# Kernel tuning notes

Measured on AMD Instinct MI355X. Metric: run time of the kernel, lower is better.

The kernel has to match this reference:

```python
import jax, jax.numpy as jnp
import numpy as np
import itertools

N = 600000
CIN = 64
COUT = 64
KS = 3
STRIDE = 2
DIL = 1
GRID = 256        # coordinate range before striding
M = 512           # per-axis key radix (fits int32 keys for batch<=2)
SHIFT = (KS - 1) // 2 * DIL   # keeps shifted coords non-negative under neighbor offsets
SENT = 2 ** 30    # sentinel key for padded unique slots
BN_EPS = 1e-5

OFFSETS = list(itertools.product(range(-(KS // 2), KS // 2 + 1), repeat=3))  # 27 offsets, row-major


def setup_inputs() -> dict:
    key = jax.random.key(0)
    k1, k2, k3, k4, k5, k6, k7, k8 = jax.random.split(key, 8)
    xyz = jax.random.randint(k1, (N, 3), 0, GRID, dtype=jnp.int32)
    b = jax.random.randint(k2, (N, 1), 0, 2, dtype=jnp.int32)  # batch of 2 scenes
    coords = jnp.concatenate([xyz, b], axis=1)                 # [N,4] = (x,y,z,batch)
    feats = jax.random.normal(k3, (N, CIN), dtype=jnp.float32)
    weight = jax.random.normal(k4, (27, CIN, COUT), dtype=jnp.float32) / np.sqrt(27 * CIN)
    bn_scale = jax.random.uniform(k5, (COUT,), jnp.float32, 0.5, 1.5)
    bn_bias = jax.random.normal(k6, (COUT,), jnp.float32) * 0.1
    bn_mean = jax.random.normal(k7, (COUT,), jnp.float32) * 0.1
    bn_var = jax.random.uniform(k8, (COUT,), jnp.float32, 0.5, 1.5)
    return {"coords": coords, "feats": feats, "weight": weight,
            "bn_scale": bn_scale, "bn_bias": bn_bias, "bn_mean": bn_mean, "bn_var": bn_var}


def _encode(xyz, b):
    # pack (batch, x, y, z) into a single sortable int32 key
    return ((b * M + xyz[:, 0] + SHIFT) * M + (xyz[:, 1] + SHIFT)) * M + (xyz[:, 2] + SHIFT)


def _forward(coords, feats, weight, bn_scale, bn_bias, bn_mean, bn_var):
    # --- stride path: voxel downsample via unique + scatter-add (index_add) ---
    xyz = coords[:, :3] // STRIDE
    b = coords[:, 3]
    keys = _encode(xyz, b)                                   # [N]
    ukeys, inv = jnp.unique(keys, size=N, fill_value=SENT, return_inverse=True)  # sorted, padded
    fds = jax.ops.segment_sum(feats, inv, num_segments=N)    # pooled feats [N, CIN]
    valid = ukeys < SENT                                      # real (non-padded) voxels

    # --- sparse 3x3x3 conv at stride 1 (output coords == input coords) ---
    # gather(neighbor) -> matmul(W_k) -> accumulate, per kernel offset
    out = jnp.zeros((N, COUT), dtype=feats.dtype)
    for k, (dx, dy, dz) in enumerate(OFFSETS):
        delta = ((dx * M) + dy) * M + dz
        q = ukeys + delta * DIL
        pos = jnp.clip(jnp.searchsorted(ukeys, q), 0, N - 1)
        match = (ukeys[pos] == q) & valid
        gathered = jnp.where(match[:, None], fds[pos], 0.0)   # [N, CIN]
        out = out + gathered @ weight[k]

    # --- BatchNorm (eval-mode running stats) + ReLU ---
    inv_std = jax.lax.rsqrt(bn_var + BN_EPS)
    out = (out - bn_mean) * (bn_scale * inv_std) + bn_bias
    out = jax.nn.relu(out)
    return jnp.where(valid[:, None], out, 0.0)                # zero padded rows


def reference(coords, feats, weight, bn_scale, bn_bias, bn_mean, bn_var):
    return _forward(coords, feats, weight, bn_scale, bn_bias, bn_mean, bn_var)
```

## Files before the change

kernel.cpp:

```cpp
#include <hip/hip_runtime.h>
#include <hip/hip_bf16.h>

#define NPTS 600000
#define NKEYS (1 << 22)
#define CHUNK 4096
#define NPART (NKEYS / CHUNK)

typedef unsigned int u32;
typedef unsigned short u16;
typedef __attribute__((ext_vector_type(8))) short short8;
typedef __attribute__((ext_vector_type(4))) float f32x4;

__device__ __forceinline__ u16 f2bf(float x) {
  union { float f; u32 u; } c; c.f = x;
  u32 r = c.u + 0x7fffu + ((c.u >> 16) & 1u);
  return (u16)(r >> 16);
}

__global__ void k0a_bn(const float* __restrict__ s, const float* __restrict__ b,
                       const float* __restrict__ m, const float* __restrict__ v,
                       float* __restrict__ ab) {
  int c = threadIdx.x;
  float a = s[c] * rsqrtf(v[c] + 1e-5f);
  ab[c] = a;
  ab[64 + c] = b[c] - m[c] * a;
}

__global__ void k0b_wt(const float* __restrict__ W, u16* __restrict__ Wt) {
  int e = blockIdx.x * 256 + threadIdx.x;
  if (e >= 27 * 4096) return;
  int k = e >> 12, rem = e & 4095, cin = rem >> 6, cout = rem & 63;
  Wt[(k << 12) + (cout << 6) + cin] = f2bf(W[e]);
}

__global__ void k1_keys(const int* __restrict__ coords, int* __restrict__ keys,
                        u32* __restrict__ lut) {
  int i = blockIdx.x * 256 + threadIdx.x;
  if (i >= NPTS) return;
  int4 c4 = *(const int4*)(coords + i * 4);
  int k = (c4.w << 21) | ((c4.x >> 1) << 14) | ((c4.y >> 1) << 7) | (c4.z >> 1);
  keys[i] = k;
  atomicAdd(&lut[k], 1u);
}

__global__ void k2a_part(const u32* __restrict__ lut, u32* __restrict__ partials) {
  __shared__ u32 sd[256];
  int blk = blockIdx.x, t = threadIdx.x;
  const u32* p = lut + blk * CHUNK;
  u32 s = 0;
  for (int j = t; j < CHUNK; j += 256) s += (p[j] != 0u);
  sd[t] = s; __syncthreads();
  for (int o = 128; o > 0; o >>= 1) { if (t < o) sd[t] += sd[t + o]; __syncthreads(); }
  if (t == 0) partials[blk] = sd[0];
}

__global__ void k2b_top(u32* __restrict__ partials) {
  __shared__ u32 sh[NPART];
  int t = threadIdx.x;
  u32 x = partials[t];
  sh[t] = x; __syncthreads();
  for (int off = 1; off < NPART; off <<= 1) {
    u32 add = (t >= off) ? sh[t - off] : 0u;
    __syncthreads();
    sh[t] += add;
    __syncthreads();
  }
  partials[t] = sh[t] - x;
  if (t == NPART - 1) partials[NPART] = sh[t];
}

__global__ void k2c_fill(u32* __restrict__ lut, const u32* __restrict__ partials,
                         int* __restrict__ r2k, float* __restrict__ fds32) {
  __shared__ u32 tsum[256];
  int blk = blockIdx.x, t = threadIdx.x;
  int base = blk * CHUNK + t * 16;
  u32 loc[16]; u32 s = 0;
#pragma unroll
  for (int j = 0; j < 16; j++) { loc[j] = lut[base + j]; s += (loc[j] != 0u); }
  tsum[t] = s; __syncthreads();
  for (int off = 1; off < 256; off <<= 1) {
    u32 add = (t >= off) ? tsum[t - off] : 0u;
    __syncthreads();
    tsum[t] += add;
    __syncthreads();
  }
  u32 rank = partials[blk] + tsum[t] - s;
#pragma unroll
  for (int j = 0; j < 16; j++) {
    if (loc[j]) {
      u32 flag = (loc[j] > 1u) ? 0x80000000u : 0u;
      lut[base + j] = (rank + 1u) | flag;
      r2k[rank] = base + j;
      if (flag) {
        float4 z = {0.f, 0.f, 0.f, 0.f};
        float* d = fds32 + ((size_t)rank << 6);
#pragma unroll
        for (int c = 0; c < 16; c++) *(float4*)(d + c * 4) = z;
      }
      rank++;
    } else lut[base + j] = 0u;
  }
}

__global__ void k3_seg(const float* __restrict__ feats, const int* __restrict__ keys,
                       const u32* __restrict__ lut, float* __restrict__ fds32,
                       u16* __restrict__ fdsb) {
  int idx = blockIdx.x * 256 + threadIdx.x;
  if (idx >= NPTS * 16) return;
  int i = idx >> 4, q = (idx & 15) << 2;
  u32 lv = lut[keys[i]];
  u32 r = (lv & 0x7fffffffu) - 1u;
  float4 v = *(const float4*)(feats + (size_t)i * 64 + q);
  if (lv >> 31) {
    float* dst = fds32 + ((size_t)r << 6) + q;
    atomicAdd(dst + 0, v.x); atomicAdd(dst + 1, v.y);
    atomicAdd(dst + 2, v.z); atomicAdd(dst + 3, v.w);
  } else {
    ushort4 o;
    o.x = f2bf(v.x); o.y = f2bf(v.y); o.z = f2bf(v.z); o.w = f2bf(v.w);
    *(ushort4*)(fdsb + ((size_t)r << 6) + q) = o;
  }
}

__global__ void k3b_fix(const int* __restrict__ r2k, const u32* __restrict__ lut,
                        const u32* __restrict__ pU,
                        const float* __restrict__ fds32, u16* __restrict__ fdsb) {
  int idx = blockIdx.x * 256 + threadIdx.x;
  int r = idx >> 2;
  if (r >= (int)(*pU)) return;
  u32 lv = lut[r2k[r]];
  if (!(lv >> 31)) return;
  int q = (idx & 3) << 4;
  const float* src = fds32 + ((size_t)r << 6) + q;
  u16* dst = fdsb + ((size_t)r << 6) + q;
#pragma unroll
  for (int j = 0; j < 4; j++) {
    float4 v = *(const float4*)(src + j * 4);
    ushort4 o;
    o.x = f2bf(v.x); o.y = f2bf(v.y); o.z = f2bf(v.z); o.w = f2bf(v.w);
    *(ushort4*)(dst + j * 4) = o;
  }
}

__global__ __launch_bounds__(320) void k4_conv(
    const u32* __restrict__ lut, const int* __restrict__ r2k,
    const u16* __restrict__ fdsb, const u16* __restrict__ Wt,
    const u32* __restrict__ pU, const float* __restrict__ ab,
    float* __restrict__ out) {
  __shared__ __align__(16) char ldsA[2][8192];
  const u32 U = *pU;
  int tid = threadIdx.x;
  int w = tid >> 6, l = tid & 63;
  int bid = blockIdx.x;
  int cpx = (int)gridDim.x >> 3;
  int swz = (bid & 7) * cpx + (bid >> 3);
  int rbase = swz * 64;

  int key = -1, x = 0, y = 0, z = 0;
  if (w == 0) {
    int r = rbase + l;
    key = ((u32)r < U) ? r2k[r] : -1;
    z = key & 127; y = (key >> 7) & 127; x = (key >> 14) & 127;
  }
  auto probe = [&](int k) -> u32 {
    int dx = k / 9 - 1, dy = (k / 3) % 3 - 1, dz = k % 3 - 1;
    int nx = x + dx, ny = y + dy, nz = z + dz;
    bool ok = (key >= 0) & ((u32)nx < 128u) & ((u32)ny < 128u) & ((u32)nz < 128u);
    int a = ok ? (key + dx * 16384 + dy * 128 + dz) : NKEYS;
    return lut[a];
  };
  auto gather = [&](int slot, u32 lvv) {
    u32 row = lvv ? ((lvv & 0x7fffffffu) - 1u) : (u32)NPTS;
    const u16* fr = fdsb + ((size_t)row << 6);
    char* dst = &ldsA[slot][l * 128];
    int r7 = l & 7;
#pragma unroll
    for (int j = 0; j < 8; j++) {
      short8 v = *(const short8*)(fr + j * 8);
      *(short8*)(dst + (((j + r7) & 7) << 4)) = v;
    }
  };

  int ct = w - 1;
  int col = l & 15, kg = l >> 4;
  f32x4 acc[4] = {};

  u32 lv_cur = 0;
  if (w == 0) {
    lv_cur = probe(0);
    gather(0, lv_cur);
    lv_cur = probe(1);
  }
  __syncthreads();

  for (int k = 0; k < 27; k++) {
    if (w == 0) {
      if (k + 1 < 27) {
        gather((k + 1) & 1, lv_cur);
        if (k + 2 < 27) lv_cur = probe(k + 2);
      }
    } else {
      const u16* wk = Wt + (k << 12) + (((ct << 4) + col) << 6) + (kg << 3);
      short8 b0 = *(const short8*)(wk);
      short8 b1 = *(const short8*)(wk + 32);
      const char* slab = &ldsA[k & 1][0];
#pragma unroll
      for (int rt = 0; rt < 4; rt++) {
        int row = (rt << 4) + col;
        const char* rp = slab + row * 128;
        int r7 = row & 7;
        short8 a0 = *(const short8*)(rp + (((kg + r7) & 7) << 4));
        short8 a1 = *(const short8*)(rp + (((kg + 4 + r7) & 7) << 4));
        acc[rt] = __builtin_amdgcn_mfma_f32_16x16x32_bf16(a0, b0, acc[rt], 0, 0, 0);
        acc[rt] = __builtin_amdgcn_mfma_f32_16x16x32_bf16(a1, b1, acc[rt], 0, 0, 0);
      }
    }
    __syncthreads();
  }

  if (w > 0) {
    int c = (ct << 4) | col;
    float al = ab[c], be = ab[64 + c];
#pragma unroll
    for (int rt = 0; rt < 4; rt++) {
#pragma unroll
      for (int i = 0; i < 4; i++) {
        int r = rbase + (rt << 4) + (kg << 2) + i;
        if (r >= NPTS) continue;
        bool valid = ((u32)r < U);
        float vv = 0.f;
        if (valid) {
          vv = fmaf(acc[rt][i], al, be);
          vv = vv > 0.f ? vv : 0.f;
        }
        out[((size_t)r << 6) + c] = vv;
      }
    }
  }
}

extern "C" void kernel_launch(void* const* d_in, const int* in_sizes, int n_in,
                              void* d_out, int out_size, void* d_ws, size_t ws_size,
                              hipStream_t stream) {
  const int*   coords = (const int*)d_in[0];
  const float* feats  = (const float*)d_in[1];
  const float* W      = (const float*)d_in[2];
  const float* bns    = (const float*)d_in[3];
  const float* bnb    = (const float*)d_in[4];
  const float* bnm    = (const float*)d_in[5];
  const float* bnv    = (const float*)d_in[6];
  float* out = (float*)d_out;

  char* ws = (char*)d_ws;
  size_t off = 0;
  auto alloc = [&](size_t bytes) -> void* {
    void* p = ws + off;
    off += (bytes + 255) & ~(size_t)255;
    return p;
  };
  u32* lut      = (u32*)alloc((size_t)(NKEYS + 1) * 4);
  u32* partials = (u32*)alloc((NPART + 8) * 4);
  int* keys     = (int*)alloc((size_t)NPTS * 4);
  int* r2k      = (int*)alloc((size_t)NPTS * 4);
  u16* fdsb     = (u16*)alloc((size_t)(NPTS + 1) * 64 * 2);
  u16* Wt       = (u16*)alloc((size_t)27 * 4096 * 2);
  float* ab     = (float*)alloc(128 * 4);
  (void)ws_size; (void)out_size; (void)n_in; (void)in_sizes;

  float* fds32 = out;

  hipMemsetAsync(lut, 0, (size_t)(NKEYS + 1) * 4, stream);
  hipMemsetAsync(fdsb + (size_t)NPTS * 64, 0, 128, stream);

  k0a_bn<<<1, 64, 0, stream>>>(bns, bnb, bnm, bnv, ab);
  k0b_wt<<<(27 * 4096 + 255) / 256, 256, 0, stream>>>(W, Wt);
  k1_keys<<<(NPTS + 255) / 256, 256, 0, stream>>>(coords, keys, lut);
  k2a_part<<<NPART, 256, 0, stream>>>(lut, partials);
  k2b_top<<<1, NPART, 0, stream>>>(partials);
  k2c_fill<<<NPART, 256, 0, stream>>>(lut, partials, r2k, fds32);
  k3_seg<<<(NPTS * 16 + 255) / 256, 256, 0, stream>>>(feats, keys, lut, fds32, fdsb);
  k3b_fix<<<(NPTS * 4 + 255) / 256, 256, 0, stream>>>(r2k, lut, partials + NPART, fds32, fdsb);
  k4_conv<<<(NPTS + 63) / 64, 320, 0, stream>>>(lut, r2k, fdsb, Wt,
                                                partials + NPART, ab, out);
}
```

Baseline: 538.3 us.

## Gather neighbor rows via direct global-to-LDS loads and use 2x2 warp tiling

The producer wave now copies gathered neighbor feature rows straight into LDS with global_load_lds, using a column-major chunk layout (1 KB per 16-byte chunk index). Before, each lane loaded 8 short8 values into registers and wrote them to a swizzled row-major LDS buffer. The four compute waves are rearranged from one 16-column tile over 64 rows each into a 2x2 tiling of 32 rows by 32 columns, which halves the A-fragment LDS reads per wave but doubles the weight loads. Launch bounds now ask for 6 blocks per CU to raise occupancy, at the risk of register pressure from the larger accumulator set.

```diff
diff --git a/kernel.cpp b/kernel.cpp
--- a/kernel.cpp
+++ b/kernel.cpp
@@ -142,7 +142,7 @@
   }
 }
 
-__global__ __launch_bounds__(320) void k4_conv(
+__global__ __launch_bounds__(320, 6) void k4_conv(
     const u32* __restrict__ lut, const int* __restrict__ r2k,
     const u16* __restrict__ fdsb, const u16* __restrict__ Wt,
     const u32* __restrict__ pU, const float* __restrict__ ab,
@@ -171,24 +171,22 @@
   };
   auto gather = [&](int slot, u32 lvv) {
     u32 row = lvv ? ((lvv & 0x7fffffffu) - 1u) : (u32)NPTS;
-    const u16* fr = fdsb + ((size_t)row << 6);
-    char* dst = &ldsA[slot][l * 128];
-    int r7 = l & 7;
-#pragma unroll
-    for (int j = 0; j < 8; j++) {
-      short8 v = *(const short8*)(fr + j * 8);
-      *(short8*)(dst + (((j + r7) & 7) << 4)) = v;
-    }
+    const char* fr = (const char*)(fdsb + ((size_t)row << 6));
+    char* slab = &ldsA[slot][0];
+#define GL(J) __builtin_amdgcn_global_load_lds( \
+      (const __attribute__((address_space(1))) void*)(fr + (J) * 16), \
+      (__attribute__((address_space(3))) void*)(slab + (J) * 1024), 16, 0, 0);
+    GL(0) GL(1) GL(2) GL(3) GL(4) GL(5) GL(6) GL(7)
+#undef GL
   };
 
-  int ct = w - 1;
+  int wi = (w - 1) >> 1, wj = (w - 1) & 1;
   int col = l & 15, kg = l >> 4;
-  f32x4 acc[4] = {};
+  f32x4 acc[2][2] = {};
 
   u32 lv_cur = 0;
   if (w == 0) {
-    lv_cur = probe(0);
-    gather(0, lv_cur);
+    gather(0, probe(0));
     lv_cur = probe(1);
   }
   __syncthreads();
@@ -200,40 +198,52 @@
         if (k + 2 < 27) lv_cur = probe(k + 2);
       }
     } else {
-      const u16* wk = Wt + (k << 12) + (((ct << 4) + col) << 6) + (kg << 3);
-      short8 b0 = *(const short8*)(wk);
-      short8 b1 = *(const short8*)(wk + 32);
+      const u16* wk = Wt + (k << 12);
+      short8 bf[2][2];
+#pragma unroll
+      for (int ct = 0; ct < 2; ct++)
+#pragma unroll
+        for (int h = 0; h < 2; h++)
+          bf[ct][h] = *(const short8*)(wk + (((wj << 5) + (ct << 4) + col) << 6) + (h << 5) + (kg << 3));
       const char* slab = &ldsA[k & 1][0];
-#pragma unroll
-      for (int rt = 0; rt < 4; rt++) {
-        int row = (rt << 4) + col;
-        const char* rp = slab + row * 128;
-        int r7 = row & 7;
-        short8 a0 = *(const short8*)(rp + (((kg + r7) & 7) << 4));
-        short8 a1 = *(const short8*)(rp + (((kg + 4 + r7) & 7) << 4));
-        acc[rt] = __builtin_amdgcn_mfma_f32_16x16x32_bf16(a0, b0, acc[rt], 0, 0, 0);
-        acc[rt] = __builtin_amdgcn_mfma_f32_16x16x32_bf16(a1, b1, acc[rt], 0, 0, 0);
-      }
+      short8 af[2][2];
+#pragma unroll
+      for (int rt = 0; rt < 2; rt++) {
+        int row = (wi << 5) + (rt << 4) + col;
+#pragma unroll
+        for (int h = 0; h < 2; h++)
+          af[rt][h] = *(const short8*)(slab + ((kg + (h << 2)) << 10) + (row << 4));
+      }
+#pragma unroll
+      for (int rt = 0; rt < 2; rt++)
+#pragma unroll
+        for (int ct = 0; ct < 2; ct++) {
+          acc[rt][ct] = __builtin_amdgcn_mfma_f32_16x16x32_bf16(af[rt][0], bf[ct][0], acc[rt][ct], 0, 0, 0);
+          acc[rt][ct] = __builtin_amdgcn_mfma_f32_16x16x32_bf16(af[rt][1], bf[ct][1], acc[rt][ct], 0, 0, 0);
+        }
     }
     __syncthreads();
   }
 
   if (w > 0) {
-    int c = (ct << 4) | col;
-    float al = ab[c], be = ab[64 + c];
-#pragma unroll
-    for (int rt = 0; rt < 4; rt++) {
-#pragma unroll
-      for (int i = 0; i < 4; i++) {
-        int r = rbase + (rt << 4) + (kg << 2) + i;
-        if (r >= NPTS) continue;
-        bool valid = ((u32)r < U);
-        float vv = 0.f;
-        if (valid) {
-          vv = fmaf(acc[rt][i], al, be);
-          vv = vv > 0.f ? vv : 0.f;
+#pragma unroll
+    for (int ct = 0; ct < 2; ct++) {
+      int c = (wj << 5) + (ct << 4) + col;
+      float al = ab[c], be = ab[64 + c];
+#pragma unroll
+      for (int rt = 0; rt < 2; rt++) {
+#pragma unroll
+        for (int i = 0; i < 4; i++) {
+          int r = rbase + (wi << 5) + (rt << 4) + (kg << 2) + i;
+          if (r >= NPTS) continue;
+          bool valid = ((u32)r < U);
+          float vv = 0.f;
+          if (valid) {
+            vv = fmaf(acc[rt][ct][i], al, be);
+            vv = vv > 0.f ? vv : 0.f;
+          }
+          out[((size_t)r << 6) + c] = vv;
         }
-        out[((size_t)r << 6) + c] = vv;
       }
     }
   }
```

Result: slower. 739.8 us (+37.4%).

## Deepen producer-wave pipeline in conv: register-staged gathers and early LUT probes

Applied to the files above, without the earlier changes.

The producer wave in the sparse conv kernel now issues LUT probes four offsets ahead and loads neighbor feature rows into registers two offsets ahead, writing them to LDS one step later. This lets the global-load latency overlap with the MFMA work of the consumer waves. The __syncthreads is replaced by an explicit lgkmcnt wait plus s_barrier so that outstanding global loads are not drained at each step. Missing neighbors are now zero-filled in registers rather than read from a zero pad row, so that memset is dropped. The cost is higher register use in the producer wave and a fully unrolled 27-step loop.

```diff
diff --git a/kernel.cpp b/kernel.cpp
--- a/kernel.cpp
+++ b/kernel.cpp
@@ -162,43 +162,52 @@
     key = ((u32)r < U) ? r2k[r] : -1;
     z = key & 127; y = (key >> 7) & 127; x = (key >> 14) & 127;
   }
-  auto probe = [&](int k) -> u32 {
-    int dx = k / 9 - 1, dy = (k / 3) % 3 - 1, dz = k % 3 - 1;
-    int nx = x + dx, ny = y + dy, nz = z + dz;
-    bool ok = (key >= 0) & ((u32)nx < 128u) & ((u32)ny < 128u) & ((u32)nz < 128u);
-    int a = ok ? (key + dx * 16384 + dy * 128 + dz) : NKEYS;
-    return lut[a];
-  };
-  auto gather = [&](int slot, u32 lvv) {
-    u32 row = lvv ? ((lvv & 0x7fffffffu) - 1u) : (u32)NPTS;
-    const u16* fr = fdsb + ((size_t)row << 6);
-    char* dst = &ldsA[slot][l * 128];
-    int r7 = l & 7;
-#pragma unroll
-    for (int j = 0; j < 8; j++) {
-      short8 v = *(const short8*)(fr + j * 8);
-      *(short8*)(dst + (((j + r7) & 7) << 4)) = v;
-    }
-  };
+  u32 lvr[4];
+  short8 rg[2][8];
+  const short8 z8 = {0, 0, 0, 0, 0, 0, 0, 0};
+
+#define PROBE(T) { \
+    const int dx_ = (T) / 9 - 1, dy_ = ((T) / 3) % 3 - 1, dz_ = (T) % 3 - 1; \
+    int nx_ = x + dx_, ny_ = y + dy_, nz_ = z + dz_; \
+    bool ok_ = (key >= 0) & ((u32)nx_ < 128u) & ((u32)ny_ < 128u) & ((u32)nz_ < 128u); \
+    int a_ = ok_ ? (key + dx_ * 16384 + dy_ * 128 + dz_) : NKEYS; \
+    lvr[(T) & 3] = lut[a_]; }
+
+#define LOADRG(T) { \
+    u32 lv_ = lvr[(T) & 3]; \
+    _Pragma("unroll") for (int j = 0; j < 8; j++) rg[(T) & 1][j] = z8; \
+    if (lv_) { \
+      const u16* fr_ = fdsb + ((size_t)((lv_ & 0x7fffffffu) - 1u) << 6); \
+      _Pragma("unroll") for (int j = 0; j < 8; j++) \
+        rg[(T) & 1][j] = *(const short8*)(fr_ + j * 8); } }
+
+#define DSW(T) { \
+    char* dst_ = &ldsA[(T) & 1][l * 128]; \
+    int r7_ = l & 7; \
+    _Pragma("unroll") for (int j = 0; j < 8; j++) \
+      *(short8*)(dst_ + (((j + r7_) & 7) << 4)) = rg[(T) & 1][j]; }
 
   int ct = w - 1;
   int col = l & 15, kg = l >> 4;
   f32x4 acc[4] = {};
 
-  u32 lv_cur = 0;
   if (w == 0) {
-    lv_cur = probe(0);
-    gather(0, lv_cur);
-    lv_cur = probe(1);
-  }
-  __syncthreads();
-
+    PROBE(0) PROBE(1) PROBE(2) PROBE(3)
+    LOADRG(0)
+    DSW(0)
+    LOADRG(1)
+  }
+  asm volatile("" ::: "memory");
+  asm volatile("s_waitcnt lgkmcnt(0)" ::: "memory");
+  __builtin_amdgcn_s_barrier();
+  asm volatile("" ::: "memory");
+
+#pragma unroll
   for (int k = 0; k < 27; k++) {
     if (w == 0) {
-      if (k + 1 < 27) {
-        gather((k + 1) & 1, lv_cur);
-        if (k + 2 < 27) lv_cur = probe(k + 2);
-      }
+      if (k + 1 < 27) DSW(k + 1)
+      if (k + 2 < 27) LOADRG(k + 2)
+      if (k + 4 < 27) PROBE(k + 4)
     } else {
       const u16* wk = Wt + (k << 12) + (((ct << 4) + col) << 6) + (kg << 3);
       short8 b0 = *(const short8*)(wk);
@@ -215,8 +224,14 @@
         acc[rt] = __builtin_amdgcn_mfma_f32_16x16x32_bf16(a1, b1, acc[rt], 0, 0, 0);
       }
     }
-    __syncthreads();
-  }
+    asm volatile("" ::: "memory");
+    asm volatile("s_waitcnt lgkmcnt(0)" ::: "memory");
+    __builtin_amdgcn_s_barrier();
+    asm volatile("" ::: "memory");
+  }
+#undef PROBE
+#undef LOADRG
+#undef DSW
 
   if (w > 0) {
     int c = (ct << 4) | col;
@@ -270,7 +285,6 @@
   float* fds32 = out;
 
   hipMemsetAsync(lut, 0, (size_t)(NKEYS + 1) * 4, stream);
-  hipMemsetAsync(fdsb + (size_t)NPTS * 64, 0, 128, stream);
 
   k0a_bn<<<1, 64, 0, stream>>>(bns, bnb, bnm, bnv, ab);
   k0b_wt<<<(27 * 4096 + 255) / 256, 256, 0, stream>>>(W, Wt);
```

Result: slower. 590.8 us (+9.8%).
